# Performance work log

Measured on AMD Instinct MI355X. Metric: run time of the kernel, lower is better.

## Reference

```python
import jax, jax.numpy as jnp
import numpy as np
from jax import lax

# dims: batch, seq len, views, d_model; d_state, d_inner=2*d_model, d_conv, dt_rank=ceil(d_model/16)
B, L, V, D = 4, 512, 4, 256
DS, DI, DCONV, DTR = 16, 512, 4, 16
EPS = 1e-5

def setup_inputs():
    key = jax.random.key(0)
    ks = jax.random.split(key, 10)
    rn = lambda k, s, sc: jax.random.normal(k, s, jnp.float32) * sc
    return {
        "x": rn(ks[0], (B, L, V, D), 1.0),
        "ln_g": jnp.ones((V, D), jnp.float32),
        "ln_b": jnp.zeros((V, D), jnp.float32),
        "w_in": rn(ks[1], (V, 2 * DI, D), D ** -0.5),
        "conv_w": rn(ks[2], (V, DI, DCONV), DCONV ** -0.5),
        "conv_b": rn(ks[3], (V, DI), 0.02),
        "w_x": rn(ks[4], (V, DTR + 2 * DS, DI), DI ** -0.5),
        "w_dt": rn(ks[5], (V, DI, DTR), DTR ** -0.5),
        "b_dt": rn(ks[6], (V, DI), 0.02),
        "A_log": rn(ks[7], (V, DI, DS), 0.5),
        "D_skip": jnp.ones((V, DI), jnp.float32),
        "w_out": rn(ks[8], (V, D, DI), DI ** -0.5),
    }

def _layernorm(x, g, b):
    mu = x.mean(-1, keepdims=True)
    var = ((x - mu) ** 2).mean(-1, keepdims=True)
    return (x - mu) * lax.rsqrt(var + EPS) * g + b

def _mamba_view(xv, w_in, conv_w, conv_b, w_x, w_dt, b_dt, A_log, D_skip, w_out):
    # xv: (B, L, D)
    xz = jnp.einsum('bld,ed->ble', xv, w_in)            # (B, L, 2*DI)
    xi, z = xz[..., :DI], xz[..., DI:]
    # causal depthwise conv over time
    xt = jnp.moveaxis(xi, 1, 2)                          # (B, DI, L)
    xt = jnp.pad(xt, ((0, 0), (0, 0), (DCONV - 1, 0)))
    xc = lax.conv_general_dilated(xt, conv_w[:, None, :], (1,), 'VALID',
                                  feature_group_count=DI,
                                  dimension_numbers=('NCH', 'OIH', 'NCH'))
    xc = jax.nn.silu(xc + conv_b[None, :, None])
    xc = jnp.moveaxis(xc, 1, 2)                          # (B, L, DI)
    xdbl = jnp.einsum('bld,ed->ble', xc, w_x)            # (B, L, DTR+2*DS)
    dt_lo = xdbl[..., :DTR]
    Bc = xdbl[..., DTR:DTR + DS]
    Cc = xdbl[..., DTR + DS:]
    delta = jax.nn.softplus(jnp.einsum('blr,dr->bld', dt_lo, w_dt) + b_dt)
    A = -jnp.exp(A_log)                                  # (DI, DS)
    dA = jnp.exp(jnp.einsum('bld,dn->bldn', delta, A))   # discretized A
    dBu = jnp.einsum('bld,bln,bld->bldn', delta, Bc, xc) # discretized B*u

    def step(h, inp):
        dA_t, dBu_t, C_t = inp
        h = dA_t * h + dBu_t                             # (B, DI, DS)
        return h, jnp.einsum('bdn,bn->bd', h, C_t)

    h0 = jnp.zeros((B, DI, DS), xv.dtype)
    _, ys = lax.scan(step, h0, (jnp.moveaxis(dA, 1, 0), jnp.moveaxis(dBu, 1, 0), jnp.moveaxis(Cc, 1, 0)))
    y = jnp.moveaxis(ys, 0, 1) + xc * D_skip             # (B, L, DI)
    y = y * jax.nn.silu(z)
    return jnp.einsum('bld,od->blo', y, w_out)           # (B, L, D)

def _forward(x, ln_g, ln_b, w_in, conv_w, conv_b, w_x, w_dt, b_dt, A_log, D_skip, w_out):
    xv = jnp.moveaxis(x, 2, 0)                           # (V, B, L, D)
    def per_view(xv_i, g, b, wi, cw, cb, wx, wdt, bdt, al, dsk, wo):
        return _mamba_view(_layernorm(xv_i, g, b), wi, cw, cb, wx, wdt, bdt, al, dsk, wo)
    outs = jax.vmap(per_view)(xv, ln_g, ln_b, w_in, conv_w, conv_b, w_x, w_dt, b_dt, A_log, D_skip, w_out)
    return jnp.moveaxis(outs, 0, 2)                      # (B, L, V, D)

def reference(x, ln_g, ln_b, w_in, conv_w, conv_b, w_x, w_dt, b_dt, A_log, D_skip, w_out):
    # eval mode: view_mask == ones, dropout identity, gather is None -> h == agents
    agents = _forward(x, ln_g, ln_b, w_in, conv_w, conv_b, w_x, w_dt, b_dt, A_log, D_skip, w_out)
    return (agents, agents)
```

## Files before the change

### kernel.cpp

```cpp
#include <hip/hip_runtime.h>
#include <hip/hip_bf16.h>
#include <math.h>

#define B_ 4
#define L_ 512
#define V_ 4
#define D_ 256
#define DS_ 16
#define DI_ 512
#define DTR_ 16
#define ML (B_*L_)
#define NC_ 16
#define CL_ 32

#define OFF_RA   0
#define SZ_RA    ((long)V_*ML*D_)
#define OFF_XZ   (OFF_RA + SZ_RA)
#define SZ_XZ    ((long)V_*ML*2*DI_)
#define OFF_XC   (OFF_XZ + SZ_XZ)
#define SZ_XC    ((long)V_*ML*DI_)
#define OFF_XDBL (OFF_XC + SZ_XC)
#define SZ_XDBL  ((long)V_*ML*48)
#define OFF_SDEL (OFF_XDBL + SZ_XDBL)
#define SZ_SDEL  ((long)V_*B_*NC_*DI_)

typedef short short8_t __attribute__((ext_vector_type(8)));
typedef float f32x4_t  __attribute__((ext_vector_type(4)));

__device__ __forceinline__ float silu_f(float x) { return x / (1.f + expf(-x)); }
__device__ __forceinline__ ushort f2bf(float f) {
    uint u = __float_as_uint(f);
    return (ushort)((u + 0x7fffu + ((u >> 16) & 1u)) >> 16);
}
__device__ __forceinline__ float bf2f(ushort h) { return __uint_as_float(((uint)h) << 16); }

__global__ __launch_bounds__(256) void split_w(const float* __restrict__ in,
                                               ushort* __restrict__ oh,
                                               ushort* __restrict__ ol, int n4)
{
    const int i = blockIdx.x*256 + threadIdx.x;
    if (i >= n4) return;
    const float4 f = ((const float4*)in)[i];
    const ushort h0=f2bf(f.x), h1=f2bf(f.y), h2=f2bf(f.z), h3=f2bf(f.w);
    ((short4*)oh)[i] = make_short4((short)h0,(short)h1,(short)h2,(short)h3);
    ((short4*)ol)[i] = make_short4((short)f2bf(f.x-bf2f(h0)), (short)f2bf(f.y-bf2f(h1)),
                                   (short)f2bf(f.z-bf2f(h2)), (short)f2bf(f.w-bf2f(h3)));
}

__global__ __launch_bounds__(256) void ln_split(const float* __restrict__ x,
                                                const float* __restrict__ g,
                                                const float* __restrict__ bta,
                                                ushort* __restrict__ xh,
                                                ushort* __restrict__ xl)
{
    const int m = blockIdx.x;
    const int v = blockIdx.y;
    const int d = threadIdx.x;
    const float val = x[((long)m*V_ + v)*D_ + d];
    float s = val, sq = val*val;
#pragma unroll
    for (int off = 32; off >= 1; off >>= 1) {
        s  += __shfl_xor(s, off);
        sq += __shfl_xor(sq, off);
    }
    __shared__ float ws[4], wq[4];
    if ((threadIdx.x & 63) == 0) { ws[threadIdx.x >> 6] = s; wq[threadIdx.x >> 6] = sq; }
    __syncthreads();
    s  = ws[0]+ws[1]+ws[2]+ws[3];
    sq = wq[0]+wq[1]+wq[2]+wq[3];
    const float mu  = s * (1.f/D_);
    const float var = sq * (1.f/D_) - mu*mu;
    const float inv = rsqrtf(var + 1e-5f);
    const float r = (val - mu)*inv*g[v*D_+d] + bta[v*D_+d];
    const ushort h = f2bf(r);
    const long idx = ((long)v*ML + m)*D_ + d;
    xh[idx] = h;
    xl[idx] = f2bf(r - bf2f(h));
}

__global__ __launch_bounds__(256,2) void mfma_gemm_in(
    const ushort* __restrict__ Ah, const ushort* __restrict__ Al,
    const ushort* __restrict__ Bh, const ushort* __restrict__ Bl,
    float* __restrict__ C)
{
    const int v = blockIdx.z;
    const long Ao = (long)v*ML*D_;
    const long Bo = (long)v*(2*DI_)*D_;
    C += (long)v*ML*(2*DI_);
    const int bm = blockIdx.y*128, bn = blockIdx.x*128;
    __shared__ ushort sAh[128][40], sAl[128][40], sBh[128][40], sBl[128][40];
    const int tid  = threadIdx.x;
    const int lane = tid & 63, w = tid >> 6;
    const int wr = w >> 1, wc = w & 1;
    const int fm = lane & 15, fg = lane >> 4;
    const int r = tid >> 1, q0 = (tid & 1)*2;

    f32x4_t acc[4][4];
#pragma unroll
    for (int i=0;i<4;++i)
#pragma unroll
        for (int j=0;j<4;++j)
#pragma unroll
            for (int k=0;k<4;++k) acc[i][j][k]=0.f;

    const ushort* Agh = Ah + Ao + (long)(bm+r)*D_ + q0*8;
    const ushort* Agl = Al + Ao + (long)(bm+r)*D_ + q0*8;
    const ushort* Bgh = Bh + Bo + (long)(bn+r)*D_ + q0*8;
    const ushort* Bgl = Bl + Bo + (long)(bn+r)*D_ + q0*8;

    for (int k0 = 0; k0 < D_; k0 += 32) {
        const uint4 a0 = *(const uint4*)(Agh + k0);
        const uint4 a1 = *(const uint4*)(Agh + k0 + 8);
        const uint4 a2 = *(const uint4*)(Agl + k0);
        const uint4 a3 = *(const uint4*)(Agl + k0 + 8);
        const uint4 b0 = *(const uint4*)(Bgh + k0);
        const uint4 b1 = *(const uint4*)(Bgh + k0 + 8);
        const uint4 b2 = *(const uint4*)(Bgl + k0);
        const uint4 b3 = *(const uint4*)(Bgl + k0 + 8);
        __syncthreads();
        *(uint4*)&sAh[r][q0*8]   = a0;  *(uint4*)&sAh[r][q0*8+8] = a1;
        *(uint4*)&sAl[r][q0*8]   = a2;  *(uint4*)&sAl[r][q0*8+8] = a3;
        *(uint4*)&sBh[r][q0*8]   = b0;  *(uint4*)&sBh[r][q0*8+8] = b1;
        *(uint4*)&sBl[r][q0*8]   = b2;  *(uint4*)&sBl[r][q0*8+8] = b3;
        __syncthreads();
        short8_t ah[4], al[4], bh[4], bl[4];
#pragma unroll
        for (int i=0;i<4;++i) {
            ah[i] = *(const short8_t*)&sAh[wr*64 + i*16 + fm][fg*8];
            al[i] = *(const short8_t*)&sAl[wr*64 + i*16 + fm][fg*8];
            bh[i] = *(const short8_t*)&sBh[wc*64 + i*16 + fm][fg*8];
            bl[i] = *(const short8_t*)&sBl[wc*64 + i*16 + fm][fg*8];
        }
#pragma unroll
        for (int i=0;i<4;++i)
#pragma unroll
            for (int j=0;j<4;++j) {
                acc[i][j] = __builtin_amdgcn_mfma_f32_16x16x32_bf16(ah[i], bh[j], acc[i][j], 0,0,0);
                acc[i][j] = __builtin_amdgcn_mfma_f32_16x16x32_bf16(ah[i], bl[j], acc[i][j], 0,0,0);
                acc[i][j] = __builtin_amdgcn_mfma_f32_16x16x32_bf16(al[i], bh[j], acc[i][j], 0,0,0);
            }
    }
#pragma unroll
    for (int i=0;i<4;++i)
#pragma unroll
        for (int j4=0;j4<4;++j4) {
            const int row = bm + wr*64 + i*16 + fg*4 + j4;
            float* cr = C + (long)row*(2*DI_) + bn + wc*64 + fm;
#pragma unroll
            for (int j=0;j<4;++j) cr[j*16] = acc[i][j][j4];
        }
}

__global__ __launch_bounds__(256,2) void mfma_gemm_out(
    const uint* __restrict__ Apk,
    const ushort* __restrict__ Bh, const ushort* __restrict__ Bl,
    float* __restrict__ Cout)
{
    const int v = blockIdx.z;
    Apk += (long)v*ML*DI_;
    const long Bo = (long)v*D_*DI_;
    const int bm = blockIdx.y*128, bn = blockIdx.x*128;
    __shared__ ushort sAh[128][40], sAl[128][40], sBh[128][40], sBl[128][40];
    const int tid  = threadIdx.x;
    const int lane = tid & 63, w = tid >> 6;
    const int wr = w >> 1, wc = w & 1;
    const int fm = lane & 15, fg = lane >> 4;
    const int r = tid >> 1, hh = tid & 1, q0 = (tid & 1)*2;

    f32x4_t acc[4][4];
#pragma unroll
    for (int i=0;i<4;++i)
#pragma unroll
        for (int j=0;j<4;++j)
#pragma unroll
            for (int k=0;k<4;++k) acc[i][j][k]=0.f;

    const uint*   Ag  = Apk + (long)(bm+r)*DI_ + hh*16;
    const ushort* Bgh = Bh + Bo + (long)(bn+r)*DI_ + q0*8;
    const ushort* Bgl = Bl + Bo + (long)(bn+r)*DI_ + q0*8;

    for (int k0 = 0; k0 < DI_; k0 += 32) {
        const uint4 p0 = *(const uint4*)(Ag + k0);
        const uint4 p1 = *(const uint4*)(Ag + k0 + 4);
        const uint4 p2 = *(const uint4*)(Ag + k0 + 8);
        const uint4 p3 = *(const uint4*)(Ag + k0 + 12);
        const uint4 b0 = *(const uint4*)(Bgh + k0);
        const uint4 b1 = *(const uint4*)(Bgh + k0 + 8);
        const uint4 b2 = *(const uint4*)(Bgl + k0);
        const uint4 b3 = *(const uint4*)(Bgl + k0 + 8);
        __syncthreads();
        *(short4*)&sAh[r][hh*16+ 0] = make_short4((short)(p0.x&0xffff),(short)(p0.y&0xffff),(short)(p0.z&0xffff),(short)(p0.w&0xffff));
        *(short4*)&sAl[r][hh*16+ 0] = make_short4((short)(p0.x>>16),(short)(p0.y>>16),(short)(p0.z>>16),(short)(p0.w>>16));
        *(short4*)&sAh[r][hh*16+ 4] = make_short4((short)(p1.x&0xffff),(short)(p1.y&0xffff),(short)(p1.z&0xffff),(short)(p1.w&0xffff));
        *(short4*)&sAl[r][hh*16+ 4] = make_short4((short)(p1.x>>16),(short)(p1.y>>16),(short)(p1.z>>16),(short)(p1.w>>16));
        *(short4*)&sAh[r][hh*16+ 8] = make_short4((short)(p2.x&0xffff),(short)(p2.y&0xffff),(short)(p2.z&0xffff),(short)(p2.w&0xffff));
        *(short4*)&sAl[r][hh*16+ 8] = make_short4((short)(p2.x>>16),(short)(p2.y>>16),(short)(p2.z>>16),(short)(p2.w>>16));
        *(short4*)&sAh[r][hh*16+12] = make_short4((short)(p3.x&0xffff),(short)(p3.y&0xffff),(short)(p3.z&0xffff),(short)(p3.w&0xffff));
        *(short4*)&sAl[r][hh*16+12] = make_short4((short)(p3.x>>16),(short)(p3.y>>16),(short)(p3.z>>16),(short)(p3.w>>16));
        *(uint4*)&sBh[r][q0*8]   = b0;  *(uint4*)&sBh[r][q0*8+8] = b1;
        *(uint4*)&sBl[r][q0*8]   = b2;  *(uint4*)&sBl[r][q0*8+8] = b3;
        __syncthreads();
        short8_t ah[4], al[4], bh[4], bl[4];
#pragma unroll
        for (int i=0;i<4;++i) {
            ah[i] = *(const short8_t*)&sAh[wr*64 + i*16 + fm][fg*8];
            al[i] = *(const short8_t*)&sAl[wr*64 + i*16 + fm][fg*8];
            bh[i] = *(const short8_t*)&sBh[wc*64 + i*16 + fm][fg*8];
            bl[i] = *(const short8_t*)&sBl[wc*64 + i*16 + fm][fg*8];
        }
#pragma unroll
        for (int i=0;i<4;++i)
#pragma unroll
            for (int j=0;j<4;++j) {
                acc[i][j] = __builtin_amdgcn_mfma_f32_16x16x32_bf16(ah[i], bh[j], acc[i][j], 0,0,0);
                acc[i][j] = __builtin_amdgcn_mfma_f32_16x16x32_bf16(ah[i], bl[j], acc[i][j], 0,0,0);
                acc[i][j] = __builtin_amdgcn_mfma_f32_16x16x32_bf16(al[i], bh[j], acc[i][j], 0,0,0);
            }
    }
    const long TOT = (long)ML * V_ * D_;
#pragma unroll
    for (int i=0;i<4;++i)
#pragma unroll
        for (int j4=0;j4<4;++j4) {
            const int row = bm + wr*64 + i*16 + fg*4 + j4;
#pragma unroll
            for (int j=0;j<4;++j) {
                const int col = bn + wc*64 + j*16 + fm;
                const long base = ((long)row*V_ + v)*D_ + col;
                const float val = acc[i][j][j4];
                Cout[base]       = val;
                Cout[base + TOT] = val;
            }
        }
}

__global__ __launch_bounds__(512) void conv_silu(const float* __restrict__ xz,
                                                 const float* __restrict__ cw,
                                                 const float* __restrict__ cb,
                                                 float* __restrict__ xc)
{
    const int m = blockIdx.x;
    const int v = blockIdx.y;
    const int c = threadIdx.x;
    const int l = m & 511;
    const float* xzv = xz + (long)v*ML*2*DI_;
    const float4 w4 = *(const float4*)&cw[((long)v*DI_ + c)*4];
    const float w[4] = {w4.x, w4.y, w4.z, w4.w};
    float acc = cb[v*DI_ + c];
#pragma unroll
    for (int k = 0; k < 4; ++k) {
        const int lp = l - 3 + k;
        if (lp >= 0) acc = fmaf(xzv[(long)(m - 3 + k)*(2*DI_) + c], w[k], acc);
    }
    xc[((long)v*ML + m)*DI_ + c] = silu_f(acc);
}

__global__ __launch_bounds__(256) void gemm_nt48(const float* __restrict__ A,
                                                 const float* __restrict__ B,
                                                 float* __restrict__ C,
                                                 int K, long sAv, long sBv, long sCv)
{
    const int v = blockIdx.z;
    A += (long)v * sAv;  B += (long)v * sBv;  C += (long)v * sCv;
    __shared__ float As[16][68];
    __shared__ float Bs[16][48];
    const int tid = threadIdx.x;
    const int tx = tid & 15, ty = tid >> 4;
    const int bm = blockIdx.y * 64;
    const int lr = tid >> 2;
    const int lk = (tid & 3) * 4;
    const float* Ag = A + (long)(bm + lr)*K + lk;
    float acc[4][3] = {};
    for (int k0 = 0; k0 < K; k0 += 16) {
        const float4 av = *(const float4*)(Ag + k0);
        float4 bv = {0,0,0,0};
        if (tid < 192) bv = *(const float4*)(B + (long)(tid >> 2)*K + k0 + (tid & 3)*4);
        __syncthreads();
        As[lk+0][lr]=av.x; As[lk+1][lr]=av.y; As[lk+2][lr]=av.z; As[lk+3][lr]=av.w;
        if (tid < 192) {
            const int br = tid >> 2, bk = (tid & 3)*4;
            Bs[bk+0][br]=bv.x; Bs[bk+1][br]=bv.y; Bs[bk+2][br]=bv.z; Bs[bk+3][br]=bv.w;
        }
        __syncthreads();
#pragma unroll
        for (int kk = 0; kk < 16; ++kk) {
            const float4 a = *(const float4*)&As[kk][ty*4];
            const float b0 = Bs[kk][tx*3+0], b1 = Bs[kk][tx*3+1], b2 = Bs[kk][tx*3+2];
            acc[0][0]=fmaf(a.x,b0,acc[0][0]); acc[0][1]=fmaf(a.x,b1,acc[0][1]); acc[0][2]=fmaf(a.x,b2,acc[0][2]);
            acc[1][0]=fmaf(a.y,b0,acc[1][0]); acc[1][1]=fmaf(a.y,b1,acc[1][1]); acc[1][2]=fmaf(a.y,b2,acc[1][2]);
            acc[2][0]=fmaf(a.z,b0,acc[2][0]); acc[2][1]=fmaf(a.z,b1,acc[2][1]); acc[2][2]=fmaf(a.z,b2,acc[2][2]);
            acc[3][0]=fmaf(a.w,b0,acc[3][0]); acc[3][1]=fmaf(a.w,b1,acc[3][1]); acc[3][2]=fmaf(a.w,b2,acc[3][2]);
        }
    }
#pragma unroll
    for (int i = 0; i < 4; ++i)
#pragma unroll
        for (int j = 0; j < 3; ++j)
            C[(long)(bm + ty*4 + i)*48 + tx*3 + j] = acc[i][j];
}

__global__ __launch_bounds__(512) void delta_kernel(const float* __restrict__ xdbl,
                                                    const float* __restrict__ wdt,
                                                    const float* __restrict__ bdt,
                                                    float* __restrict__ xz)
{
    const int m = blockIdx.x;
    const int v = blockIdx.y;
    const int d = threadIdx.x;
    const float* xd = xdbl + ((long)v*ML + m)*48;
    const float* wr = wdt + ((long)v*DI_ + d)*DTR_;
    float acc = bdt[v*DI_ + d];
#pragma unroll
    for (int r = 0; r < 16; ++r) acc = fmaf(xd[r], wr[r], acc);
    const float sp = fmaxf(acc, 0.f) + log1pf(expf(-fabsf(acc)));
    xz[((long)v*ML + m)*(2*DI_) + d] = sp;
}

__global__ __launch_bounds__(256) void scanA(const float* __restrict__ xz,
                                             const float* __restrict__ xcin,
                                             const float* __restrict__ xdbl,
                                             const float* __restrict__ A_log,
                                             float* __restrict__ hbuf,
                                             float* __restrict__ sdel)
{
    const int c = blockIdx.x >> 1, half = blockIdx.x & 1;
    const int b = blockIdx.y, v = blockIdx.z;
    const int d = half*256 + threadIdx.x;
    const long rowbase = (long)v*ML + (long)b*L_ + (long)c*CL_;
    const float* xzv = xz   + rowbase*(2*DI_);
    const float* xcv = xcin + rowbase*DI_;
    const float* xdv = xdbl + rowbase*48;

    __shared__ float sB[CL_][16];
    {
        int t = threadIdx.x;
        sB[t>>4][t&15] = xdv[(long)(t>>4)*48 + 16 + (t&15)];
        t += 256;
        sB[t>>4][t&15] = xdv[(long)(t>>4)*48 + 16 + (t&15)];
    }
    float a2[16];
#pragma unroll
    for (int n = 0; n < 16; ++n)
        a2[n] = -expf(A_log[((long)v*DI_ + d)*DS_ + n]) * 1.44269504088896341f;
    float h[16];
#pragma unroll
    for (int n = 0; n < 16; ++n) h[n] = 0.f;
    float sd = 0.f;
    __syncthreads();

    for (int g = 0; g < CL_; g += 8) {
        float dl[8], xr[8];
#pragma unroll
        for (int s = 0; s < 8; ++s) {
            dl[s] = xzv[(long)(g+s)*(2*DI_) + d];
            xr[s] = xcv[(long)(g+s)*DI_ + d];
        }
#pragma unroll
        for (int s = 0; s < 8; ++s) {
            const float delta = dl[s];
            const float t1 = delta * xr[s];
            sd += delta;
#pragma unroll
            for (int n = 0; n < 16; ++n)
                h[n] = fmaf(exp2f(delta*a2[n]), h[n], t1*sB[g+s][n]);
        }
    }
    float* hb = hbuf + ((((long)v*B_ + b)*NC_ + c)*DI_ + d)*16;
#pragma unroll
    for (int n = 0; n < 16; n += 4) {
        float4 r; r.x = h[n]; r.y = h[n+1]; r.z = h[n+2]; r.w = h[n+3];
        *(float4*)&hb[n] = r;
    }
    sdel[(((long)v*B_ + b)*NC_ + c)*DI_ + d] = sd;
}

__global__ __launch_bounds__(256) void scanB(const float* __restrict__ A_log,
                                             const float* __restrict__ sdel,
                                             float* __restrict__ hbuf)
{
    const long lin = (long)blockIdx.x*256 + threadIdx.x;
    const int n = (int)(lin & 15);
    const int d = (int)((lin >> 4) & 511);
    const int b = (int)((lin >> 13) & 3);
    const int v = (int)(lin >> 15);
    const float a2 = -expf(A_log[((long)v*DI_ + d)*DS_ + n]) * 1.44269504088896341f;
    float h = 0.f;
    long hidx = ((long)(v*B_ + b)*NC_)*DI_*16 + (long)d*16 + n;
    long sidx = ((long)(v*B_ + b)*NC_)*DI_ + d;
#pragma unroll
    for (int c = 0; c < NC_; ++c) {
        const float he = hbuf[hidx];
        const float P  = exp2f(a2 * sdel[sidx]);
        hbuf[hidx] = h;
        h = fmaf(P, h, he);
        hidx += (long)DI_*16;
        sidx += DI_;
    }
}

__global__ __launch_bounds__(256) void scanC(const float* __restrict__ xz,
                                             const float* __restrict__ xcin,
                                             const float* __restrict__ xdbl,
                                             const float* __restrict__ A_log,
                                             const float* __restrict__ D_skip,
                                             const float* __restrict__ hbuf,
                                             float* __restrict__ yout)
{
    const int c = blockIdx.x >> 1, half = blockIdx.x & 1;
    const int b = blockIdx.y, v = blockIdx.z;
    const int d = half*256 + threadIdx.x;
    const long rowbase = (long)v*ML + (long)b*L_ + (long)c*CL_;
    const float* xzv = xz   + rowbase*(2*DI_);
    const float* xcv = xcin + rowbase*DI_;
    const float* xdv = xdbl + rowbase*48;
    uint*        yv  = (uint*)yout + rowbase*DI_;

    __shared__ float sBC[CL_][32];
    for (int t = threadIdx.x; t < CL_*32; t += 256)
        sBC[t>>5][t&31] = xdv[(long)(t>>5)*48 + 16 + (t&31)];

    float a2[16];
#pragma unroll
    for (int n = 0; n < 16; ++n)
        a2[n] = -expf(A_log[((long)v*DI_ + d)*DS_ + n]) * 1.44269504088896341f;
    const float dsk = D_skip[v*DI_ + d];
    float h[16];
    const float* hb = hbuf + ((((long)v*B_ + b)*NC_ + c)*DI_ + d)*16;
#pragma unroll
    for (int n = 0; n < 16; n += 4) {
        const float4 r = *(const float4*)&hb[n];
        h[n] = r.x; h[n+1] = r.y; h[n+2] = r.z; h[n+3] = r.w;
    }
    __syncthreads();

    for (int g = 0; g < CL_; g += 8) {
        float dl[8], xr[8], zr[8];
#pragma unroll
        for (int s = 0; s < 8; ++s) {
            dl[s] = xzv[(long)(g+s)*(2*DI_) + d];
            zr[s] = xzv[(long)(g+s)*(2*DI_) + DI_ + d];
            xr[s] = xcv[(long)(g+s)*DI_ + d];
        }
#pragma unroll
        for (int s = 0; s < 8; ++s) {
            const float delta = dl[s], xcval = xr[s];
            const float t1 = delta * xcval;
            float ys = 0.f;
#pragma unroll
            for (int n = 0; n < 16; ++n) {
                const float e = exp2f(delta*a2[n]);
                h[n] = fmaf(e, h[n], t1*sBC[g+s][n]);
                ys   = fmaf(h[n], sBC[g+s][16+n], ys);
            }
            float outv = ys + xcval * dsk;
            outv *= silu_f(zr[s]);
            const ushort hv = f2bf(outv);
            const ushort lv = f2bf(outv - bf2f(hv));
            yv[(long)(g+s)*DI_ + d] = (uint)hv | ((uint)lv << 16);
        }
    }
}

extern "C" void kernel_launch(void* const* d_in, const int* in_sizes, int n_in,
                              void* d_out, int out_size, void* d_ws, size_t ws_size,
                              hipStream_t stream)
{
    const float* x      = (const float*)d_in[0];
    const float* ln_g   = (const float*)d_in[1];
    const float* ln_b   = (const float*)d_in[2];
    const float* w_in   = (const float*)d_in[3];
    const float* conv_w = (const float*)d_in[4];
    const float* conv_b = (const float*)d_in[5];
    const float* w_x    = (const float*)d_in[6];
    const float* w_dt   = (const float*)d_in[7];
    const float* b_dt   = (const float*)d_in[8];
    const float* A_log  = (const float*)d_in[9];
    const float* D_skip = (const float*)d_in[10];
    const float* w_out  = (const float*)d_in[11];
    float* out = (float*)d_out;

    float* ws   = (float*)d_ws;
    float* xz   = ws + OFF_XZ;
    float* xc   = ws + OFF_XC;
    float* xdbl = ws + OFF_XDBL;
    float* sdel = ws + OFF_SDEL;
    float* hbuf = ws + OFF_RA;

    ushort* xlnh = (ushort*)(ws + OFF_RA);
    ushort* xlnl = xlnh + (long)V_*ML*D_;
    ushort* wih = (ushort*)(ws + OFF_XC);
    ushort* wil = wih + (long)V_*(2*DI_)*D_;
    ushort* woh = (ushort*)(ws + OFF_RA);
    ushort* wol = woh + (long)V_*D_*DI_;

    split_w<<<dim3((V_*(2*DI_)*D_/4 + 255)/256), 256, 0, stream>>>(w_in, wih, wil, V_*(2*DI_)*D_/4);

    ln_split<<<dim3(ML, V_), 256, 0, stream>>>(x, ln_g, ln_b, xlnh, xlnl);

    mfma_gemm_in<<<dim3((2*DI_)/128, ML/128, V_), 256, 0, stream>>>(xlnh, xlnl, wih, wil, xz);

    conv_silu<<<dim3(ML, V_), DI_, 0, stream>>>(xz, conv_w, conv_b, xc);

    gemm_nt48<<<dim3(1, ML/64, V_), 256, 0, stream>>>(
        xc, w_x, xdbl, DI_, (long)ML*DI_, (long)48*DI_, (long)ML*48);

    delta_kernel<<<dim3(ML, V_), DI_, 0, stream>>>(xdbl, w_dt, b_dt, xz);

    scanA<<<dim3(NC_*2, B_, V_), 256, 0, stream>>>(xz, xc, xdbl, A_log, hbuf, sdel);
    scanB<<<dim3((V_*B_*DI_*DS_)/256), 256, 0, stream>>>(A_log, sdel, hbuf);
    scanC<<<dim3(NC_*2, B_, V_), 256, 0, stream>>>(xz, xc, xdbl, A_log, D_skip, hbuf, xc);

    split_w<<<dim3((V_*D_*DI_/4 + 255)/256), 256, 0, stream>>>(w_out, woh, wol, V_*D_*DI_/4);

    mfma_gemm_out<<<dim3(D_/128, ML/128, V_), 256, 0, stream>>>((const uint*)xc, woh, wol, out);
}
```

Baseline: 271.4 us.

## Split-K the x_proj GEMM and fuse dt projection and softplus into scans

The 48-wide x_proj GEMM is split along K into four slices. Each slice writes partial sums into the free x half of the xz buffer, and a small reduce kernel adds them, which gives more blocks to run in parallel. The separate delta kernel is removed. scanA and scanC now recompute the dt projection and softplus from the staged xdbl row and per-thread w_dt registers, which drops the delta write and its re-read in both scans. Register prefetch of the next eight xc and z rows is added, at the cost of recomputing delta twice and more register pressure.

```diff
diff --git a/kernel.cpp b/kernel.cpp
--- a/kernel.cpp
+++ b/kernel.cpp
@@ -255,26 +255,29 @@
     xc[((long)v*ML + m)*DI_ + c] = silu_f(acc);
 }
 
-__global__ __launch_bounds__(256) void gemm_nt48(const float* __restrict__ A,
-                                                 const float* __restrict__ B,
-                                                 float* __restrict__ C,
-                                                 int K, long sAv, long sBv, long sCv)
+__global__ __launch_bounds__(256) void gemm_nt48_sk(const float* __restrict__ A,
+                                                    const float* __restrict__ Bm,
+                                                    float* __restrict__ P,
+                                                    long sAv, long sBv)
 {
     const int v = blockIdx.z;
-    A += (long)v * sAv;  B += (long)v * sBv;  C += (long)v * sCv;
+    const int ks = blockIdx.y;
+    A  += (long)v * sAv;
+    Bm += (long)v * sBv;
+    P  += (long)v * ((long)ML*2*DI_);
     __shared__ float As[16][68];
     __shared__ float Bs[16][48];
     const int tid = threadIdx.x;
     const int tx = tid & 15, ty = tid >> 4;
-    const int bm = blockIdx.y * 64;
+    const int bm = blockIdx.x * 64;
     const int lr = tid >> 2;
     const int lk = (tid & 3) * 4;
-    const float* Ag = A + (long)(bm + lr)*K + lk;
+    const float* Ag = A + (long)(bm + lr)*DI_ + lk;
     float acc[4][3] = {};
-    for (int k0 = 0; k0 < K; k0 += 16) {
+    for (int k0 = ks*128; k0 < ks*128 + 128; k0 += 16) {
         const float4 av = *(const float4*)(Ag + k0);
         float4 bv = {0,0,0,0};
-        if (tid < 192) bv = *(const float4*)(B + (long)(tid >> 2)*K + k0 + (tid & 3)*4);
+        if (tid < 192) bv = *(const float4*)(Bm + (long)(tid >> 2)*DI_ + k0 + (tid & 3)*4);
         __syncthreads();
         As[lk+0][lr]=av.x; As[lk+1][lr]=av.y; As[lk+2][lr]=av.z; As[lk+3][lr]=av.w;
         if (tid < 192) {
@@ -296,30 +299,24 @@
     for (int i = 0; i < 4; ++i)
 #pragma unroll
         for (int j = 0; j < 3; ++j)
-            C[(long)(bm + ty*4 + i)*48 + tx*3 + j] = acc[i][j];
-}
-
-__global__ __launch_bounds__(512) void delta_kernel(const float* __restrict__ xdbl,
-                                                    const float* __restrict__ wdt,
-                                                    const float* __restrict__ bdt,
-                                                    float* __restrict__ xz)
-{
-    const int m = blockIdx.x;
-    const int v = blockIdx.y;
-    const int d = threadIdx.x;
-    const float* xd = xdbl + ((long)v*ML + m)*48;
-    const float* wr = wdt + ((long)v*DI_ + d)*DTR_;
-    float acc = bdt[v*DI_ + d];
-#pragma unroll
-    for (int r = 0; r < 16; ++r) acc = fmaf(xd[r], wr[r], acc);
-    const float sp = fmaxf(acc, 0.f) + log1pf(expf(-fabsf(acc)));
-    xz[((long)v*ML + m)*(2*DI_) + d] = sp;
-}
-
-__global__ __launch_bounds__(256) void scanA(const float* __restrict__ xz,
-                                             const float* __restrict__ xcin,
+            P[(long)(bm + ty*4 + i)*(2*DI_) + ks*48 + tx*3 + j] = acc[i][j];
+}
+
+__global__ __launch_bounds__(256) void reduce48(const float* __restrict__ xz,
+                                                float* __restrict__ xdbl)
+{
+    const long i = (long)blockIdx.x*256 + threadIdx.x;
+    if (i >= (long)V_*ML*48) return;
+    const long row = i / 48; const int j = (int)(i % 48);
+    const float* p = xz + row*(2*DI_);
+    xdbl[i] = (p[j] + p[48+j]) + (p[96+j] + p[144+j]);
+}
+
+__global__ __launch_bounds__(256) void scanA(const float* __restrict__ xcin,
                                              const float* __restrict__ xdbl,
                                              const float* __restrict__ A_log,
+                                             const float* __restrict__ wdt,
+                                             const float* __restrict__ bdt,
                                              float* __restrict__ hbuf,
                                              float* __restrict__ sdel)
 {
@@ -327,43 +324,56 @@
     const int b = blockIdx.y, v = blockIdx.z;
     const int d = half*256 + threadIdx.x;
     const long rowbase = (long)v*ML + (long)b*L_ + (long)c*CL_;
-    const float* xzv = xz   + rowbase*(2*DI_);
     const float* xcv = xcin + rowbase*DI_;
     const float* xdv = xdbl + rowbase*48;
 
-    __shared__ float sB[CL_][16];
-    {
-        int t = threadIdx.x;
-        sB[t>>4][t&15] = xdv[(long)(t>>4)*48 + 16 + (t&15)];
-        t += 256;
-        sB[t>>4][t&15] = xdv[(long)(t>>4)*48 + 16 + (t&15)];
-    }
+    __shared__ float sX[CL_*48];
+    for (int t = threadIdx.x; t < CL_*48; t += 256) sX[t] = xdv[t];
+
     float a2[16];
 #pragma unroll
     for (int n = 0; n < 16; ++n)
         a2[n] = -expf(A_log[((long)v*DI_ + d)*DS_ + n]) * 1.44269504088896341f;
+    float wreg[16];
+    {
+        const float* wp = wdt + ((long)v*DI_ + d)*DTR_;
+#pragma unroll
+        for (int r = 0; r < 16; r += 4) {
+            const float4 t4 = *(const float4*)(wp + r);
+            wreg[r]=t4.x; wreg[r+1]=t4.y; wreg[r+2]=t4.z; wreg[r+3]=t4.w;
+        }
+    }
+    const float bias = bdt[(long)v*DI_ + d];
     float h[16];
 #pragma unroll
     for (int n = 0; n < 16; ++n) h[n] = 0.f;
-    float sd = 0.f;
+    float sdsum = 0.f;
     __syncthreads();
 
+    float xcur[8], xnxt[8];
+#pragma unroll
+    for (int s = 0; s < 8; ++s) xcur[s] = xcv[(long)s*DI_ + d];
+
     for (int g = 0; g < CL_; g += 8) {
-        float dl[8], xr[8];
+        if (g + 8 < CL_) {
+#pragma unroll
+            for (int s = 0; s < 8; ++s) xnxt[s] = xcv[(long)(g+8+s)*DI_ + d];
+        }
 #pragma unroll
         for (int s = 0; s < 8; ++s) {
-            dl[s] = xzv[(long)(g+s)*(2*DI_) + d];
-            xr[s] = xcv[(long)(g+s)*DI_ + d];
-        }
-#pragma unroll
-        for (int s = 0; s < 8; ++s) {
-            const float delta = dl[s];
-            const float t1 = delta * xr[s];
-            sd += delta;
+            const float* xrow = &sX[(g+s)*48];
+            float acc = bias;
+#pragma unroll
+            for (int r = 0; r < 16; ++r) acc = fmaf(xrow[r], wreg[r], acc);
+            const float delta = fmaxf(acc, 0.f) + log1pf(expf(-fabsf(acc)));
+            const float t1 = delta * xcur[s];
+            sdsum += delta;
 #pragma unroll
             for (int n = 0; n < 16; ++n)
-                h[n] = fmaf(exp2f(delta*a2[n]), h[n], t1*sB[g+s][n]);
-        }
+                h[n] = fmaf(exp2f(delta*a2[n]), h[n], t1*xrow[16+n]);
+        }
+#pragma unroll
+        for (int s = 0; s < 8; ++s) xcur[s] = xnxt[s];
     }
     float* hb = hbuf + ((((long)v*B_ + b)*NC_ + c)*DI_ + d)*16;
 #pragma unroll
@@ -371,7 +381,7 @@
         float4 r; r.x = h[n]; r.y = h[n+1]; r.z = h[n+2]; r.w = h[n+3];
         *(float4*)&hb[n] = r;
     }
-    sdel[(((long)v*B_ + b)*NC_ + c)*DI_ + d] = sd;
+    sdel[(((long)v*B_ + b)*NC_ + c)*DI_ + d] = sdsum;
 }
 
 __global__ __launch_bounds__(256) void scanB(const float* __restrict__ A_log,
@@ -402,6 +412,8 @@
                                              const float* __restrict__ xcin,
                                              const float* __restrict__ xdbl,
                                              const float* __restrict__ A_log,
+                                             const float* __restrict__ wdt,
+                                             const float* __restrict__ bdt,
                                              const float* __restrict__ D_skip,
                                              const float* __restrict__ hbuf,
                                              float* __restrict__ yout)
@@ -415,14 +427,23 @@
     const float* xdv = xdbl + rowbase*48;
     uint*        yv  = (uint*)yout + rowbase*DI_;
 
-    __shared__ float sBC[CL_][32];
-    for (int t = threadIdx.x; t < CL_*32; t += 256)
-        sBC[t>>5][t&31] = xdv[(long)(t>>5)*48 + 16 + (t&31)];
+    __shared__ float sX[CL_*48];
+    for (int t = threadIdx.x; t < CL_*48; t += 256) sX[t] = xdv[t];
 
     float a2[16];
 #pragma unroll
     for (int n = 0; n < 16; ++n)
         a2[n] = -expf(A_log[((long)v*DI_ + d)*DS_ + n]) * 1.44269504088896341f;
+    float wreg[16];
+    {
+        const float* wp = wdt + ((long)v*DI_ + d)*DTR_;
+#pragma unroll
+        for (int r = 0; r < 16; r += 4) {
+            const float4 t4 = *(const float4*)(wp + r);
+            wreg[r]=t4.x; wreg[r+1]=t4.y; wreg[r+2]=t4.z; wreg[r+3]=t4.w;
+        }
+    }
+    const float bias = bdt[(long)v*DI_ + d];
     const float dsk = D_skip[v*DI_ + d];
     float h[16];
     const float* hb = hbuf + ((((long)v*B_ + b)*NC_ + c)*DI_ + d)*16;
@@ -433,31 +454,45 @@
     }
     __syncthreads();
 
+    float xcur[8], zcur[8], xnxt[8], znxt[8];
+#pragma unroll
+    for (int s = 0; s < 8; ++s) {
+        xcur[s] = xcv[(long)s*DI_ + d];
+        zcur[s] = xzv[(long)s*(2*DI_) + DI_ + d];
+    }
+
     for (int g = 0; g < CL_; g += 8) {
-        float dl[8], xr[8], zr[8];
+        if (g + 8 < CL_) {
+#pragma unroll
+            for (int s = 0; s < 8; ++s) {
+                xnxt[s] = xcv[(long)(g+8+s)*DI_ + d];
+                znxt[s] = xzv[(long)(g+8+s)*(2*DI_) + DI_ + d];
+            }
+        }
 #pragma unroll
         for (int s = 0; s < 8; ++s) {
-            dl[s] = xzv[(long)(g+s)*(2*DI_) + d];
-            zr[s] = xzv[(long)(g+s)*(2*DI_) + DI_ + d];
-            xr[s] = xcv[(long)(g+s)*DI_ + d];
-        }
-#pragma unroll
-        for (int s = 0; s < 8; ++s) {
-            const float delta = dl[s], xcval = xr[s];
+            const float* xrow = &sX[(g+s)*48];
+            float acc = bias;
+#pragma unroll
+            for (int r = 0; r < 16; ++r) acc = fmaf(xrow[r], wreg[r], acc);
+            const float delta = fmaxf(acc, 0.f) + log1pf(expf(-fabsf(acc)));
+            const float xcval = xcur[s];
             const float t1 = delta * xcval;
             float ys = 0.f;
 #pragma unroll
             for (int n = 0; n < 16; ++n) {
                 const float e = exp2f(delta*a2[n]);
-                h[n] = fmaf(e, h[n], t1*sBC[g+s][n]);
-                ys   = fmaf(h[n], sBC[g+s][16+n], ys);
+                h[n] = fmaf(e, h[n], t1*xrow[16+n]);
+                ys   = fmaf(h[n], xrow[32+n], ys);
             }
             float outv = ys + xcval * dsk;
-            outv *= silu_f(zr[s]);
+            outv *= silu_f(zcur[s]);
             const ushort hv = f2bf(outv);
             const ushort lv = f2bf(outv - bf2f(hv));
             yv[(long)(g+s)*DI_ + d] = (uint)hv | ((uint)lv << 16);
         }
+#pragma unroll
+        for (int s = 0; s < 8; ++s) { xcur[s] = xnxt[s]; zcur[s] = znxt[s]; }
     }
 }
 
@@ -501,14 +536,14 @@
 
     conv_silu<<<dim3(ML, V_), DI_, 0, stream>>>(xz, conv_w, conv_b, xc);
 
-    gemm_nt48<<<dim3(1, ML/64, V_), 256, 0, stream>>>(
-        xc, w_x, xdbl, DI_, (long)ML*DI_, (long)48*DI_, (long)ML*48);
-
-    delta_kernel<<<dim3(ML, V_), DI_, 0, stream>>>(xdbl, w_dt, b_dt, xz);
-
-    scanA<<<dim3(NC_*2, B_, V_), 256, 0, stream>>>(xz, xc, xdbl, A_log, hbuf, sdel);
+    gemm_nt48_sk<<<dim3(ML/64, 4, V_), 256, 0, stream>>>(
+        xc, w_x, xz, (long)ML*DI_, (long)48*DI_);
+    reduce48<<<dim3((V_*ML*48 + 255)/256), 256, 0, stream>>>(xz, xdbl);
+
+    scanA<<<dim3(NC_*2, B_, V_), 256, 0, stream>>>(xc, xdbl, A_log, w_dt, b_dt, hbuf, sdel);
     scanB<<<dim3((V_*B_*DI_*DS_)/256), 256, 0, stream>>>(A_log, sdel, hbuf);
-    scanC<<<dim3(NC_*2, B_, V_), 256, 0, stream>>>(xz, xc, xdbl, A_log, D_skip, hbuf, xc);
+    scanC<<<dim3(NC_*2, B_, V_), 256, 0, stream>>>(xz, xc, xdbl, A_log, w_dt, b_dt,
+                                                   D_skip, hbuf, xc);
 
     split_w<<<dim3((V_*D_*DI_/4 + 255)/256), 256, 0, stream>>>(w_out, woh, wol, V_*D_*DI_/4);
 
```

Result: faster. 266.0 us (-2.0%).
